# Optimization experiments

Measured on AMD Instinct MI355X. Metric: run time of the kernel, lower is better.

The kernel has to match this reference:

```python
import jax, jax.numpy as jnp
import numpy as np

B, S, IN, OUT = 64, 512, 256, 256   # batch, seq_len, in/out features
R, NB, E = 40, 3, 262144            # num_rels, num_bases, num_edges
N = B * S                           # total nodes in batched graph


def setup_inputs() -> dict:
    key = jax.random.key(0)
    ks = jax.random.split(key, 6)
    text = jax.random.normal(ks[0], (B, S, IN), jnp.float32)
    src = jax.random.randint(ks[1], (E,), 0, N)
    dst = jax.random.randint(ks[2], (E,), 0, N)
    rel = jax.random.randint(ks[3], (E,), 0, R)
    bases = jax.random.normal(ks[4], (NB, IN, OUT), jnp.float32) / np.sqrt(IN).astype(np.float32)
    comp = jax.random.normal(ks[5], (R, NB), jnp.float32)
    bias = jnp.zeros((OUT,), jnp.float32)
    return dict(text=text, src=src, dst=dst, rel=rel, bases=bases, comp=comp, bias=bias)


def reference(text, src, dst, rel, bases, comp, bias):
    Bt, St, INt = text.shape
    h = text.reshape(-1, INt)                       # [N, in] flattened node feats
    n_nodes = h.shape[0]
    # project every node through every basis once: [N, num_bases, out]
    t = jnp.einsum('ni,bio->nbo', h, bases)
    # per-edge message: sum_b comp[rel_e, b] * (h_src @ basis_b)  -> [E, out]
    msg = jnp.einsum('eb,ebo->eo', comp[rel], t[src])
    # scatter-sum aggregation to destination nodes
    agg = jax.ops.segment_sum(msg, dst, num_segments=n_nodes)   # [N, out]
    out = jax.nn.relu(agg + bias)
    return out.reshape(Bt, -1, out.shape[-1])
```

## Files before the change

### kernel.cpp

```cpp
#include <hip/hip_runtime.h>
#include <cstdint>

#define N_NODES 32768
#define IN_F    256
#define OUT_F   256
#define NBASES  3
#define N_EDGES 262144
#define K_DIM   (NBASES * IN_F)

typedef __attribute__((ext_vector_type(8))) short bf16x8;
typedef __attribute__((ext_vector_type(4))) float f32x4;

__device__ __forceinline__ unsigned short f2bf(float x) {
    union { float f; unsigned int u; } c; c.f = x;
    unsigned int u = c.u;
    u = (u + 0x7FFFu + ((u >> 16) & 1u)) >> 16;
    return (unsigned short)u;
}

__device__ __forceinline__ void async_copy16(const void* g, void* l) {
    __builtin_amdgcn_global_load_lds(
        (const __attribute__((address_space(1))) unsigned int*)g,
        (__attribute__((address_space(3))) unsigned int*)l, 16, 0, 0);
}

__global__ __launch_bounds__(256) void hist_kernel(
    const int* __restrict__ dst, int* __restrict__ counts)
{
    int e = blockIdx.x * 256 + threadIdx.x;
    atomicAdd(&counts[dst[e]], 1);
}

__global__ __launch_bounds__(1024) void scan_kernel(
    int* __restrict__ counts,
    int* __restrict__ offsets)
{
    __shared__ int wsum[16];
    const int tid = threadIdx.x;
    const int wave = tid >> 6, lane = tid & 63;
    const int base = tid * 32;
    int local[32];
    int sum = 0;
    #pragma unroll
    for (int k = 0; k < 32; ++k) { local[k] = counts[base + k]; sum += local[k]; }
    int inc = sum;
    #pragma unroll
    for (int off = 1; off < 64; off <<= 1) {
        int v = __shfl_up(inc, off);
        if (lane >= off) inc += v;
    }
    if (lane == 63) wsum[wave] = inc;
    __syncthreads();
    if (wave == 0 && lane < 16) {
        int v = wsum[lane];
        #pragma unroll
        for (int off = 1; off < 16; off <<= 1) {
            int u = __shfl_up(v, off);
            if (lane >= off) v += u;
        }
        wsum[lane] = v;
    }
    __syncthreads();
    int run = inc - sum + (wave ? wsum[wave - 1] : 0);
    #pragma unroll
    for (int k = 0; k < 32; ++k) {
        offsets[base + k] = run;
        counts[base + k] = run;
        run += local[k];
    }
    if (tid == 1023) offsets[N_NODES] = run;
}

__global__ __launch_bounds__(256) void scatter_kernel(
    const int* __restrict__ dst, const int* __restrict__ src,
    const int* __restrict__ rel, int* __restrict__ cursor,
    int* __restrict__ packed)
{
    int e = blockIdx.x * 256 + threadIdx.x;
    int pos = atomicAdd(&cursor[dst[e]], 1);
    packed[pos] = (rel[e] << 16) | src[e];
}

__global__ __launch_bounds__(256) void agg_kernel(
    const float* __restrict__ h,
    const int* __restrict__ packed,
    const int* __restrict__ offsets,
    const float* __restrict__ comp,
    unsigned short* __restrict__ z)
{
    __shared__ float compS[128];
    if (threadIdx.x < 120) compS[threadIdx.x] = comp[threadIdx.x];
    __syncthreads();

    const int node = blockIdx.x * 4 + (threadIdx.x >> 6);
    const int lane = threadIdx.x & 63;
    const int start = offsets[node];
    const int end   = offsets[node + 1];

    float a0[4] = {}, a1[4] = {}, a2[4] = {};

    for (int cb = start; cb < end; cb += 64) {
        int idx = cb + lane;
        int pv = (idx < end) ? packed[idx] : 0;
        int cnt = min(64, end - cb);
        for (int j = 0; j < cnt; ++j) {
            int p = __shfl(pv, j);
            int s = p & 0xFFFF;
            int r = p >> 16;
            float c0 = compS[r * 3 + 0];
            float c1 = compS[r * 3 + 1];
            float c2 = compS[r * 3 + 2];
            float4 v = *reinterpret_cast<const float4*>(
                h + (size_t)s * IN_F + lane * 4);
            a0[0] += c0 * v.x; a0[1] += c0 * v.y; a0[2] += c0 * v.z; a0[3] += c0 * v.w;
            a1[0] += c1 * v.x; a1[1] += c1 * v.y; a1[2] += c1 * v.z; a1[3] += c1 * v.w;
            a2[0] += c2 * v.x; a2[1] += c2 * v.y; a2[2] += c2 * v.z; a2[3] += c2 * v.w;
        }
    }

    unsigned short* zp = z + (size_t)node * K_DIM + lane * 4;
    ushort4 o;
    o.x = f2bf(a0[0]); o.y = f2bf(a0[1]); o.z = f2bf(a0[2]); o.w = f2bf(a0[3]);
    *reinterpret_cast<ushort4*>(zp) = o;
    o.x = f2bf(a1[0]); o.y = f2bf(a1[1]); o.z = f2bf(a1[2]); o.w = f2bf(a1[3]);
    *reinterpret_cast<ushort4*>(zp + 256) = o;
    o.x = f2bf(a2[0]); o.y = f2bf(a2[1]); o.z = f2bf(a2[2]); o.w = f2bf(a2[3]);
    *reinterpret_cast<ushort4*>(zp + 512) = o;
}

__global__ __launch_bounds__(256) void gemm_kernel(
    const unsigned short* __restrict__ A,
    const float* __restrict__ Wf,
    const float* __restrict__ bias,
    float* __restrict__ out)
{
    constexpr int BK  = 32;
    constexpr int LDK = 40;
    __shared__ __align__(16) unsigned short As[128 * 32];
    __shared__ unsigned short Bs[128 * LDK];

    const int tid  = threadIdx.x;
    const int wave = tid >> 6, lane = tid & 63;
    const int quad = lane >> 4, l16 = lane & 15;
    const int wm = (wave & 1) * 64, wn = (wave >> 1) * 64;
    const int m0 = blockIdx.x * 128, n0 = blockIdx.y * 128;

    f32x4 acc[4][4] = {};

    const unsigned short* ga[2];
    unsigned short* la[2];
    #pragma unroll
    for (int c = 0; c < 2; ++c) {
        int p = c * 256 + wave * 64 + lane;
        int row = p >> 2;
        int oct = (p & 3) ^ ((row >> 1) & 3);
        ga[c] = A + (size_t)(m0 + row) * K_DIM + oct * 8;
        la[c] = As + (size_t)(c * 256 + wave * 64) * 8;
    }

    const int bk = tid >> 5;
    const int bn = (tid & 31) * 4;
    const int bswz = (bn >> 2) & 3;

    for (int k0 = 0; k0 < K_DIM; k0 += BK) {
        async_copy16(ga[0] + k0, la[0]);
        async_copy16(ga[1] + k0, la[1]);
        #pragma unroll
        for (int it = 0; it < 4; ++it) {
            int kk = bk + it * 8;
            float4 v = *reinterpret_cast<const float4*>(
                Wf + (size_t)(k0 + kk) * OUT_F + n0 + bn);
            int kcol = (((kk >> 3) ^ bswz) << 3) + (kk & 7);
            Bs[(bn + 0) * LDK + kcol] = f2bf(v.x);
            Bs[(bn + 1) * LDK + kcol] = f2bf(v.y);
            Bs[(bn + 2) * LDK + kcol] = f2bf(v.z);
            Bs[(bn + 3) * LDK + kcol] = f2bf(v.w);
        }
        __syncthreads();

        bf16x8 af[4], bfr[4];
        #pragma unroll
        for (int i = 0; i < 4; ++i) {
            int row = wm + i * 16 + l16;
            int oph = quad ^ ((row >> 1) & 3);
            af[i] = *reinterpret_cast<const bf16x8*>(&As[(row * 4 + oph) * 8]);
            int nn  = wn + i * 16 + l16;
            int oct = quad ^ ((nn >> 2) & 3);
            bfr[i] = *reinterpret_cast<const bf16x8*>(&Bs[nn * LDK + oct * 8]);
        }
        #pragma unroll
        for (int i = 0; i < 4; ++i)
            #pragma unroll
            for (int j = 0; j < 4; ++j)
                acc[i][j] = __builtin_amdgcn_mfma_f32_16x16x32_bf16(
                    af[i], bfr[j], acc[i][j], 0, 0, 0);
        __syncthreads();
    }

    #pragma unroll
    for (int j = 0; j < 4; ++j) {
        int col = n0 + wn + j * 16 + l16;
        float bv = bias[col];
        #pragma unroll
        for (int i = 0; i < 4; ++i) {
            int row_base = m0 + wm + i * 16 + quad * 4;
            #pragma unroll
            for (int r = 0; r < 4; ++r)
                out[(size_t)(row_base + r) * OUT_F + col] =
                    fmaxf(acc[i][j][r] + bv, 0.f);
        }
    }
}

extern "C" void kernel_launch(void* const* d_in, const int* in_sizes, int n_in,
                              void* d_out, int out_size, void* d_ws, size_t ws_size,
                              hipStream_t stream) {
    const float* text  = (const float*)d_in[0];
    const int*   src   = (const int*)d_in[1];
    const int*   dst   = (const int*)d_in[2];
    const int*   rel   = (const int*)d_in[3];
    const float* bases = (const float*)d_in[4];
    const float* comp  = (const float*)d_in[5];
    const float* bias  = (const float*)d_in[6];
    float* out = (float*)d_out;

    unsigned short* z = (unsigned short*)d_ws;
    int* packed  = (int*)((char*)d_ws + (size_t)N_NODES * K_DIM * 2);
    int* offsets = packed + N_EDGES;
    int* counts  = offsets + (N_NODES + 1);

    hipMemsetAsync(counts, 0, (size_t)N_NODES * sizeof(int), stream);

    hist_kernel<<<N_EDGES / 256, 256, 0, stream>>>(dst, counts);
    scan_kernel<<<1, 1024, 0, stream>>>(counts, offsets);
    scatter_kernel<<<N_EDGES / 256, 256, 0, stream>>>(dst, src, rel, counts, packed);
    agg_kernel<<<N_NODES / 4, 256, 0, stream>>>(text, packed, offsets, comp, z);
    gemm_kernel<<<dim3(N_NODES / 128, OUT_F / 128), 256, 0, stream>>>(
        z, bases, bias, out);
}
```

Baseline: 215.3 us.

## Pre-convert features and bases to bf16; async-load transposed weights in GEMM

A new prep kernel converts node features to bf16 and transposes the bases into a bf16 [OUT, K] layout. The aggregation kernel can then gather half-width rows, processing two edges per iteration, and the GEMM loads B tiles with async global-to-LDS copies instead of converting fp32 on the fly. This targets the gather bandwidth in aggregation and the per-tile conversion overhead in the GEMM. The cost is an extra pass over the features, extra workspace, and bf16 rounding of inputs before accumulation, with a fallback to the fp32 path when the workspace is too small.

```diff
diff --git a/kernel.cpp b/kernel.cpp
--- a/kernel.cpp
+++ b/kernel.cpp
@@ -17,11 +17,48 @@
     u = (u + 0x7FFFu + ((u >> 16) & 1u)) >> 16;
     return (unsigned short)u;
 }
+__device__ __forceinline__ float bf2f(unsigned short h) {
+    union { unsigned int u; float f; } c; c.u = ((unsigned int)h) << 16;
+    return c.f;
+}
 
 __device__ __forceinline__ void async_copy16(const void* g, void* l) {
     __builtin_amdgcn_global_load_lds(
         (const __attribute__((address_space(1))) unsigned int*)g,
         (__attribute__((address_space(3))) unsigned int*)l, 16, 0, 0);
+}
+
+__global__ __launch_bounds__(256) void prep_kernel(
+    const float* __restrict__ text,
+    const float* __restrict__ bases,
+    unsigned short* __restrict__ hb,
+    unsigned short* __restrict__ Wt)
+{
+    const int tid = threadIdx.x;
+    if (blockIdx.x < 8192) {
+        if (!hb) return;
+        int i = blockIdx.x * 256 + tid;
+        float4 v = reinterpret_cast<const float4*>(text)[i];
+        ushort4 o;
+        o.x = f2bf(v.x); o.y = f2bf(v.y); o.z = f2bf(v.z); o.w = f2bf(v.w);
+        reinterpret_cast<ushort4*>(hb)[i] = o;
+    } else {
+        int tb = blockIdx.x - 8192;
+        int kb = tb % 24, ob = tb / 24;
+        __shared__ float tile[32][33];
+        int c = tid & 31, r8 = tid >> 5;
+        #pragma unroll
+        for (int i = 0; i < 4; ++i) {
+            int r = r8 + 8 * i;
+            tile[r][c] = bases[(size_t)(kb * 32 + r) * OUT_F + ob * 32 + c];
+        }
+        __syncthreads();
+        #pragma unroll
+        for (int i = 0; i < 4; ++i) {
+            int r = r8 + 8 * i;
+            Wt[(size_t)(ob * 32 + r) * K_DIM + kb * 32 + c] = f2bf(tile[c][r]);
+        }
+    }
 }
 
 __global__ __launch_bounds__(256) void hist_kernel(
@@ -81,8 +118,8 @@
     packed[pos] = (rel[e] << 16) | src[e];
 }
 
-__global__ __launch_bounds__(256) void agg_kernel(
-    const float* __restrict__ h,
+__global__ __launch_bounds__(256) void agg_bf16_kernel(
+    const unsigned short* __restrict__ hb,
     const int* __restrict__ packed,
     const int* __restrict__ offsets,
     const float* __restrict__ comp,
@@ -103,18 +140,40 @@
         int idx = cb + lane;
         int pv = (idx < end) ? packed[idx] : 0;
         int cnt = min(64, end - cb);
-        for (int j = 0; j < cnt; ++j) {
-            int p = __shfl(pv, j);
-            int s = p & 0xFFFF;
-            int r = p >> 16;
-            float c0 = compS[r * 3 + 0];
-            float c1 = compS[r * 3 + 1];
-            float c2 = compS[r * 3 + 2];
-            float4 v = *reinterpret_cast<const float4*>(
-                h + (size_t)s * IN_F + lane * 4);
-            a0[0] += c0 * v.x; a0[1] += c0 * v.y; a0[2] += c0 * v.z; a0[3] += c0 * v.w;
-            a1[0] += c1 * v.x; a1[1] += c1 * v.y; a1[2] += c1 * v.z; a1[3] += c1 * v.w;
-            a2[0] += c2 * v.x; a2[1] += c2 * v.y; a2[2] += c2 * v.z; a2[3] += c2 * v.w;
+        int j = 0;
+        for (; j + 2 <= cnt; j += 2) {
+            int p0 = __shfl(pv, j);
+            int p1 = __shfl(pv, j + 1);
+            int s0 = p0 & 0xFFFF, r0 = p0 >> 16;
+            int s1 = p1 & 0xFFFF, r1 = p1 >> 16;
+            ushort4 u0 = *reinterpret_cast<const ushort4*>(
+                hb + (size_t)s0 * IN_F + lane * 4);
+            ushort4 u1 = *reinterpret_cast<const ushort4*>(
+                hb + (size_t)s1 * IN_F + lane * 4);
+            float c00 = compS[r0*3], c01 = compS[r0*3+1], c02 = compS[r0*3+2];
+            float c10 = compS[r1*3], c11 = compS[r1*3+1], c12 = compS[r1*3+2];
+            float v0[4] = { bf2f(u0.x), bf2f(u0.y), bf2f(u0.z), bf2f(u0.w) };
+            float v1[4] = { bf2f(u1.x), bf2f(u1.y), bf2f(u1.z), bf2f(u1.w) };
+            #pragma unroll
+            for (int k = 0; k < 4; ++k) {
+                a0[k] += c00 * v0[k] + c10 * v1[k];
+                a1[k] += c01 * v0[k] + c11 * v1[k];
+                a2[k] += c02 * v0[k] + c12 * v1[k];
+            }
+        }
+        if (j < cnt) {
+            int p0 = __shfl(pv, j);
+            int s0 = p0 & 0xFFFF, r0 = p0 >> 16;
+            ushort4 u0 = *reinterpret_cast<const ushort4*>(
+                hb + (size_t)s0 * IN_F + lane * 4);
+            float c00 = compS[r0*3], c01 = compS[r0*3+1], c02 = compS[r0*3+2];
+            float v0[4] = { bf2f(u0.x), bf2f(u0.y), bf2f(u0.z), bf2f(u0.w) };
+            #pragma unroll
+            for (int k = 0; k < 4; ++k) {
+                a0[k] += c00 * v0[k];
+                a1[k] += c01 * v0[k];
+                a2[k] += c02 * v0[k];
+            }
         }
     }
 
@@ -128,16 +187,54 @@
     *reinterpret_cast<ushort4*>(zp + 512) = o;
 }
 
+__global__ __launch_bounds__(256) void agg_f32_kernel(
+    const float* __restrict__ h,
+    const int* __restrict__ packed,
+    const int* __restrict__ offsets,
+    const float* __restrict__ comp,
+    unsigned short* __restrict__ z)
+{
+    __shared__ float compS[128];
+    if (threadIdx.x < 120) compS[threadIdx.x] = comp[threadIdx.x];
+    __syncthreads();
+    const int node = blockIdx.x * 4 + (threadIdx.x >> 6);
+    const int lane = threadIdx.x & 63;
+    const int start = offsets[node];
+    const int end   = offsets[node + 1];
+    float a0[4] = {}, a1[4] = {}, a2[4] = {};
+    for (int cb = start; cb < end; cb += 64) {
+        int idx = cb + lane;
+        int pv = (idx < end) ? packed[idx] : 0;
+        int cnt = min(64, end - cb);
+        for (int j = 0; j < cnt; ++j) {
+            int p = __shfl(pv, j);
+            int s = p & 0xFFFF, r = p >> 16;
+            float c0 = compS[r*3], c1 = compS[r*3+1], c2 = compS[r*3+2];
+            float4 v = *reinterpret_cast<const float4*>(
+                h + (size_t)s * IN_F + lane * 4);
+            a0[0] += c0*v.x; a0[1] += c0*v.y; a0[2] += c0*v.z; a0[3] += c0*v.w;
+            a1[0] += c1*v.x; a1[1] += c1*v.y; a1[2] += c1*v.z; a1[3] += c1*v.w;
+            a2[0] += c2*v.x; a2[1] += c2*v.y; a2[2] += c2*v.z; a2[3] += c2*v.w;
+        }
+    }
+    unsigned short* zp = z + (size_t)node * K_DIM + lane * 4;
+    ushort4 o;
+    o.x = f2bf(a0[0]); o.y = f2bf(a0[1]); o.z = f2bf(a0[2]); o.w = f2bf(a0[3]);
+    *reinterpret_cast<ushort4*>(zp) = o;
+    o.x = f2bf(a1[0]); o.y = f2bf(a1[1]); o.z = f2bf(a1[2]); o.w = f2bf(a1[3]);
+    *reinterpret_cast<ushort4*>(zp + 256) = o;
+    o.x = f2bf(a2[0]); o.y = f2bf(a2[1]); o.z = f2bf(a2[2]); o.w = f2bf(a2[3]);
+    *reinterpret_cast<ushort4*>(zp + 512) = o;
+}
+
 __global__ __launch_bounds__(256) void gemm_kernel(
     const unsigned short* __restrict__ A,
-    const float* __restrict__ Wf,
+    const unsigned short* __restrict__ Bt,
     const float* __restrict__ bias,
     float* __restrict__ out)
 {
-    constexpr int BK  = 32;
-    constexpr int LDK = 40;
     __shared__ __align__(16) unsigned short As[128 * 32];
-    __shared__ unsigned short Bs[128 * LDK];
+    __shared__ __align__(16) unsigned short Bs[128 * 32];
 
     const int tid  = threadIdx.x;
     const int wave = tid >> 6, lane = tid & 63;
@@ -147,35 +244,24 @@
 
     f32x4 acc[4][4] = {};
 
-    const unsigned short* ga[2];
-    unsigned short* la[2];
+    const unsigned short *ga[2], *gb[2];
+    unsigned short *la[2], *lb[2];
     #pragma unroll
     for (int c = 0; c < 2; ++c) {
         int p = c * 256 + wave * 64 + lane;
         int row = p >> 2;
         int oct = (p & 3) ^ ((row >> 1) & 3);
-        ga[c] = A + (size_t)(m0 + row) * K_DIM + oct * 8;
+        ga[c] = A  + (size_t)(m0 + row) * K_DIM + oct * 8;
+        gb[c] = Bt + (size_t)(n0 + row) * K_DIM + oct * 8;
         la[c] = As + (size_t)(c * 256 + wave * 64) * 8;
-    }
-
-    const int bk = tid >> 5;
-    const int bn = (tid & 31) * 4;
-    const int bswz = (bn >> 2) & 3;
-
-    for (int k0 = 0; k0 < K_DIM; k0 += BK) {
+        lb[c] = Bs + (size_t)(c * 256 + wave * 64) * 8;
+    }
+
+    for (int k0 = 0; k0 < K_DIM; k0 += 32) {
         async_copy16(ga[0] + k0, la[0]);
         async_copy16(ga[1] + k0, la[1]);
-        #pragma unroll
-        for (int it = 0; it < 4; ++it) {
-            int kk = bk + it * 8;
-            float4 v = *reinterpret_cast<const float4*>(
-                Wf + (size_t)(k0 + kk) * OUT_F + n0 + bn);
-            int kcol = (((kk >> 3) ^ bswz) << 3) + (kk & 7);
-            Bs[(bn + 0) * LDK + kcol] = f2bf(v.x);
-            Bs[(bn + 1) * LDK + kcol] = f2bf(v.y);
-            Bs[(bn + 2) * LDK + kcol] = f2bf(v.z);
-            Bs[(bn + 3) * LDK + kcol] = f2bf(v.w);
-        }
+        async_copy16(gb[0] + k0, lb[0]);
+        async_copy16(gb[1] + k0, lb[1]);
         __syncthreads();
 
         bf16x8 af[4], bfr[4];
@@ -184,9 +270,9 @@
             int row = wm + i * 16 + l16;
             int oph = quad ^ ((row >> 1) & 3);
             af[i] = *reinterpret_cast<const bf16x8*>(&As[(row * 4 + oph) * 8]);
-            int nn  = wn + i * 16 + l16;
-            int oct = quad ^ ((nn >> 2) & 3);
-            bfr[i] = *reinterpret_cast<const bf16x8*>(&Bs[nn * LDK + oct * 8]);
+            int nn   = wn + i * 16 + l16;
+            int oph2 = quad ^ ((nn >> 1) & 3);
+            bfr[i] = *reinterpret_cast<const bf16x8*>(&Bs[(nn * 4 + oph2) * 8]);
         }
         #pragma unroll
         for (int i = 0; i < 4; ++i)
@@ -224,17 +310,25 @@
     const float* bias  = (const float*)d_in[6];
     float* out = (float*)d_out;
 
-    unsigned short* z = (unsigned short*)d_ws;
-    int* packed  = (int*)((char*)d_ws + (size_t)N_NODES * K_DIM * 2);
-    int* offsets = packed + N_EDGES;
-    int* counts  = offsets + (N_NODES + 1);
+    char* p = (char*)d_ws;
+    unsigned short* z = (unsigned short*)p;       p += (size_t)N_NODES * K_DIM * 2;
+    int* packed  = (int*)p;                       p += (size_t)N_EDGES * 4;
+    int* offsets = (int*)p;                       p += (size_t)(N_NODES + 4) * 4;
+    int* counts  = (int*)p;                       p += (size_t)N_NODES * 4;
+    unsigned short* Wt = (unsigned short*)p;      p += (size_t)OUT_F * K_DIM * 2;
+    bool use_bf16_h = (ws_size >= (size_t)(p - (char*)d_ws) + (size_t)N_NODES * IN_F * 2);
+    unsigned short* hb = use_bf16_h ? (unsigned short*)p : nullptr;
 
     hipMemsetAsync(counts, 0, (size_t)N_NODES * sizeof(int), stream);
 
+    prep_kernel<<<8384, 256, 0, stream>>>(text, bases, hb, Wt);
     hist_kernel<<<N_EDGES / 256, 256, 0, stream>>>(dst, counts);
     scan_kernel<<<1, 1024, 0, stream>>>(counts, offsets);
     scatter_kernel<<<N_EDGES / 256, 256, 0, stream>>>(dst, src, rel, counts, packed);
-    agg_kernel<<<N_NODES / 4, 256, 0, stream>>>(text, packed, offsets, comp, z);
+    if (use_bf16_h)
+        agg_bf16_kernel<<<N_NODES / 4, 256, 0, stream>>>(hb, packed, offsets, comp, z);
+    else
+        agg_f32_kernel<<<N_NODES / 4, 256, 0, stream>>>(text, packed, offsets, comp, z);
     gemm_kernel<<<dim3(N_NODES / 128, OUT_F / 128), 256, 0, stream>>>(
-        z, bases, bias, out);
-}
+        z, Wt, bias, out);
+}
```

Result: faster. 187.8 us (-12.8%).
